# Kernel optimization log

Hardware: AMD Instinct MI355X
Metric: run time of the kernel (lower is better)

The kernel has to match this reference:

```python
import jax, jax.numpy as jnp
import numpy as np

B, S, D_MODEL, H, OUT = 32, 64, 256, 256, 10
N_POS = 64  # n_max_seq + 1


def _coordinate_map():
    i = jnp.arange(N_POS, dtype=jnp.float32)
    r = jnp.sqrt(jnp.float32(N_POS))
    c0 = (i / r - 2.0) / 2.0
    c1 = (jnp.mod(i, r) - 2.0) / 2.0
    coord = jnp.stack([c0, c1], axis=-1)            # [N_POS, 2]
    return jnp.broadcast_to(coord[None], (B, N_POS, 2))


def setup_inputs() -> dict:
    key = jax.random.key(0)
    ks = jax.random.split(key, 13)
    d_in = (D_MODEL + 2) * 3
    w = lambda k, i, o: jax.random.normal(k, (i, o), jnp.float32) * 0.02
    b = lambda k, o: jax.random.normal(k, (o,), jnp.float32) * 0.02
    return {
        'sentences': jax.random.normal(ks[0], (B, S, D_MODEL), jnp.float32),
        'coord': _coordinate_map(),
        'g_w1': w(ks[1], d_in, H), 'g_b1': b(ks[2], H),
        'g_w2': w(ks[3], H, H),    'g_b2': b(ks[4], H),
        'g_w3': w(ks[5], H, H),    'g_b3': b(ks[6], H),
        'f_w1': w(ks[7], H, H),    'f_b1': b(ks[8], H),
        'f_w2': w(ks[9], H, H),    'f_b2': b(ks[10], H),
        'f_w3': w(ks[11], H, OUT), 'f_b3': b(ks[12], OUT),
    }


def reference(sentences, coord, g_w1, g_b1, g_w2, g_b2, g_w3, g_b3,
              f_w1, f_b1, f_w2, f_b2, f_w3, f_b3):
    b, s, d = sentences.shape
    x = jnp.concatenate([sentences, coord[:b, :s, :]], axis=-1)   # [B,S,D+2]
    oi = jnp.broadcast_to(x[:, None, :, :], (b, s, s, d + 2))     # object_i[b,i,j]=x[b,j]
    oj = jnp.broadcast_to(x[:, :, None, :], (b, s, s, d + 2))     # object_j[b,i,j]=x[b,i]
    pairs = jnp.concatenate([oi, oj, oi * oj], axis=-1)           # [B,S,S,3*(D+2)]
    h = jax.nn.relu(jnp.einsum('bijk,kh->bijh', pairs, g_w1) + g_b1)
    h = jax.nn.relu(h @ g_w2 + g_b2)
    h = jax.nn.relu(h @ g_w3 + g_b3)
    rel = h.reshape(b, s * s, -1).sum(axis=1)                     # [B,H]
    y = jax.nn.relu(rel @ f_w1 + f_b1)
    y = jax.nn.relu(y @ f_w2 + f_b2)                              # Dropout: eval mode (identity)
    return y @ f_w3 + f_b3                                        # [B,OUT]
```

## Files before the change

### kernel.cpp

```cpp
#include <hip/hip_runtime.h>
#include <hip/hip_bf16.h>


typedef __attribute__((ext_vector_type(4))) float f32x4;
typedef __attribute__((ext_vector_type(16))) float f32x16;
typedef __attribute__((ext_vector_type(8))) short frag8;
typedef __attribute__((ext_vector_type(4))) unsigned u32x4;

__device__ __forceinline__ float bf2f(short s) {
  return __uint_as_float(((unsigned)(unsigned short)s) << 16);
}
__device__ __forceinline__ short f2bf(float f) {
  unsigned u = __float_as_uint(f);
  return (short)((u + 0x7fffu + ((u >> 16) & 1u)) >> 16);
}

__device__ __forceinline__ unsigned pk_bf16(float lo, float hi) {
#if __has_builtin(__builtin_amdgcn_cvt_pk_bf16_f32)
  return __builtin_bit_cast(unsigned, __builtin_amdgcn_cvt_pk_bf16_f32(lo, hi));
#else
  unsigned ul = __float_as_uint(lo), uh = __float_as_uint(hi);
  ul = (ul + 0x7fffu + ((ul >> 16) & 1u)) >> 16;
  uh = (uh + 0x7fffu + ((uh >> 16) & 1u)) & 0xffff0000u;
  return ul | uh;
#endif
}

__device__ __forceinline__ unsigned pk_mul_bf16(unsigned a, unsigned b) {
  float al = __uint_as_float(a << 16);
  float ah = __uint_as_float(a & 0xffff0000u);
  float bl = __uint_as_float(b << 16);
  float bh = __uint_as_float(b & 0xffff0000u);
  return pk_bf16(al * bl, ah * bh);
}

__device__ __forceinline__ frag8 pk_mul4(u32x4 a, u32x4 b) {
  u32x4 r;
#pragma unroll
  for (int t = 0; t < 4; t++) r[t] = pk_mul_bf16(a[t], b[t]);
  return __builtin_bit_cast(frag8, r);
}

#define KX 288

__global__ __launch_bounds__(256)
void prep(const float* __restrict__ sent, const float* __restrict__ coord,
          const float* __restrict__ g_w1, const float* __restrict__ g_w2,
          const float* __restrict__ g_w3,
          short* __restrict__ xb, short* __restrict__ Wab, short* __restrict__ Wc,
          short* __restrict__ W2t, short* __restrict__ W3t, float* __restrict__ rel) {
  __shared__ short tile[64 * 66];
  const int blk = blockIdx.x, t = threadIdx.x;

  if (blk < 288) {
    long idx0 = ((long)blk * 256 + t) * 8;
#pragma unroll
    for (int e = 0; e < 8; e++) {
      long idx = idx0 + e;
      int row = (int)(idx / KX), k = (int)(idx - (long)row * KX);
      float v = 0.f;
      if (k < 256)      v = sent[(size_t)row * 256 + k];
      else if (k < 258) v = coord[row * 2 + (k - 256)];
      xb[idx] = f2bf(v);
    }
    return;
  }

  const int nc = t & 63, r4 = t >> 6;
  if (blk < 328) {
    int tt = blk - 288, kt = tt >> 3, nt = tt & 7;
    int k0 = kt * 64, n0 = nt * 64;
    for (int p = 0; p < 16; p++) {
      int kl = p * 4 + r4, k = k0 + kl, n = n0 + nc;
      float v = 0.f;
      if (k < 258) {
        int row = (n < 256) ? k : 258 + k;
        int col = (n < 256) ? n : n - 256;
        v = g_w1[(size_t)row * 256 + col];
      }
      tile[kl * 66 + nc] = f2bf(v);
    }
    __syncthreads();
    for (int p = 0; p < 16; p++) {
      int nl = p * 4 + r4;
      if (k0 + nc < KX) Wab[(size_t)(n0 + nl) * KX + k0 + nc] = tile[nc * 66 + nl];
    }
    return;
  }
  if (blk < 348) {
    int tt = blk - 328, kt = tt >> 2, nt = tt & 3;
    int k0 = kt * 64, n0 = nt * 64;
    for (int p = 0; p < 16; p++) {
      int kl = p * 4 + r4, k = k0 + kl;
      float v = (k < 258) ? g_w1[(size_t)(516 + k) * 256 + n0 + nc] : 0.f;
      tile[kl * 66 + nc] = f2bf(v);
    }
    __syncthreads();
    for (int p = 0; p < 16; p++) {
      int nl = p * 4 + r4;
      if (k0 + nc < KX) Wc[(size_t)(n0 + nl) * KX + k0 + nc] = tile[nc * 66 + nl];
    }
    return;
  }
  if (blk < 380) {
    int tt = blk - 348;
    const float* W = (tt < 16) ? g_w2 : g_w3;
    short* Wt = (tt < 16) ? W2t : W3t;
    tt &= 15;
    int k0 = (tt >> 2) * 64, n0 = (tt & 3) * 64;
    for (int p = 0; p < 16; p++) {
      int kl = p * 4 + r4;
      tile[kl * 66 + nc] = f2bf(W[(size_t)(k0 + kl) * 256 + n0 + nc]);
    }
    __syncthreads();
    for (int p = 0; p < 16; p++) {
      int nl = p * 4 + r4;
      Wt[(size_t)(n0 + nl) * 256 + k0 + nc] = tile[nc * 66 + nl];
    }
    return;
  }
  {
    int bb = blk - 380;
    ((f32x4*)rel)[bb * 256 + t] = (f32x4){0.f, 0.f, 0.f, 0.f};
  }
}


__global__ __launch_bounds__(64)
void uv_gemm(const short* __restrict__ xb, const short* __restrict__ Wab,
             const float* __restrict__ g_b1, float* __restrict__ uv) {
  const int m0 = blockIdx.x * 64;
  const int n0 = blockIdx.y * 64;
  const int lane = threadIdx.x;
  const int q = lane >> 4, l16 = lane & 15;

  f32x4 acc[4][4];
#pragma unroll
  for (int mt = 0; mt < 4; mt++)
#pragma unroll
    for (int nt = 0; nt < 4; nt++) acc[mt][nt] = (f32x4){0.f, 0.f, 0.f, 0.f};

  for (int k0 = 0; k0 < KX; k0 += 32) {
    frag8 a[4], bb[4];
#pragma unroll
    for (int mt = 0; mt < 4; mt++)
      a[mt] = *(const frag8*)(xb + (size_t)(m0 + mt * 16 + l16) * KX + k0 + q * 8);
#pragma unroll
    for (int nt = 0; nt < 4; nt++)
      bb[nt] = *(const frag8*)(Wab + (size_t)(n0 + nt * 16 + l16) * KX + k0 + q * 8);
#pragma unroll
    for (int mt = 0; mt < 4; mt++)
#pragma unroll
      for (int nt = 0; nt < 4; nt++)
        acc[mt][nt] = __builtin_amdgcn_mfma_f32_16x16x32_bf16(a[mt], bb[nt], acc[mt][nt], 0, 0, 0);
  }
#pragma unroll
  for (int nt = 0; nt < 4; nt++) {
    int col = n0 + nt * 16 + l16;
    float bias = (col >= 256) ? g_b1[col - 256] : 0.f;
#pragma unroll
    for (int mt = 0; mt < 4; mt++) {
      int m = m0 + mt * 16 + q * 4;
#pragma unroll
      for (int r = 0; r < 4; r++)
        uv[(size_t)(m + r) * 512 + col] = acc[mt][nt][r] + bias;
    }
  }
}


#define ASH 152
#define A2OFF (128 * ASH)
#define LDS_SHORTS (2 * 128 * ASH)

__global__ __launch_bounds__(512, 4)
void relnet_main(const short* __restrict__ xb, const short* __restrict__ Wc,
                 const short* __restrict__ W2t, const short* __restrict__ W3t,
                 const float* __restrict__ uv, const float* __restrict__ g_b2,
                 const float* __restrict__ g_b3, float* __restrict__ rel) {
  __shared__ short lds[LDS_SHORTS];

  const int tid = threadIdx.x;
  const int bi = blockIdx.x;
  const int b = bi >> 5, ip = bi & 31;
  const int i0 = ip * 2;
  const int lane = tid & 63, wave = tid >> 6;
  const int l32 = lane & 31, half = lane >> 5;
  const int n0 = wave * 32;
  const int rowbase = b * 64;
  const int swr = l32 & 7;
  const int col = n0 + l32;
  const int cb = n0 >> 3;

  f32x16 acc[4];
#pragma unroll
  for (int mt = 0; mt < 4; mt++)
#pragma unroll
    for (int r = 0; r < 16; r++) acc[mt][r] = 0.f;

#pragma unroll
  for (int it = 0; it < 9; it++) {
    int idx = tid + it * 512;
    if (idx < 4352) {
      int j = idx / 34, c = idx - j * 34;
      int k = c * 8;
      u32x4 aj = *(const u32x4*)(xb + (size_t)(rowbase + (j & 63)) * KX + k);
      u32x4 ai = *(const u32x4*)(xb + (size_t)(rowbase + i0 + (j >> 6)) * KX + k);
      frag8 pr = pk_mul4(aj, ai);
      if (c < 18) *(frag8*)(&lds[j * ASH + k]) = pr;
      else        *(frag8*)(&lds[A2OFF + j * ASH + (k - 144)]) = pr;
    }
  }
  __syncthreads();

  {
    const short* wc = Wc + (size_t)(n0 + l32) * KX + half * 8;
    frag8 b0 = *(const frag8*)(wc);
#pragma unroll
    for (int ks = 0; ks < 17; ks++) {
      frag8 b1;
      if (ks < 16) b1 = *(const frag8*)(wc + (ks + 1) * 16);
      frag8 a[4];
#pragma unroll
      for (int mt = 0; mt < 4; mt++) {
        int base = (ks < 9) ? ((mt * 32 + l32) * ASH + ks * 16 + half * 8)
                            : (A2OFF + (mt * 32 + l32) * ASH + (ks - 9) * 16 + half * 8);
        a[mt] = *(const frag8*)(&lds[base]);
      }
#pragma unroll
      for (int mt = 0; mt < 4; mt++)
        acc[mt] = __builtin_amdgcn_mfma_f32_32x32x16_bf16(a[mt], b0, acc[mt], 0, 0, 0);
      b0 = b1;
    }
  }
  __syncthreads();

  {
    const float* ub = uv + (size_t)rowbase * 512;
    float vv0 = uv[(size_t)(rowbase + i0) * 512 + 256 + col];
    float vv1 = uv[(size_t)(rowbase + i0 + 1) * 512 + 256 + col];
#pragma unroll
    for (int mt = 0; mt < 4; mt++) {
      float vv = (mt < 2) ? vv0 : vv1;
#pragma unroll
      for (int r = 0; r < 16; r += 2) {
        int rb0 = (r & 3) + 8 * (r >> 2) + 4 * half;
        int jm0 = (mt & 1) * 32 + rb0;
        float x0 = fmaxf(acc[mt][r]     + ub[(size_t)jm0 * 512 + col] + vv, 0.f);
        float x1 = fmaxf(acc[mt][r + 1] + ub[(size_t)(jm0 + 1) * 512 + col] + vv, 0.f);
        unsigned pk = pk_bf16(x0, x1);
        int m0r = mt * 32 + rb0;
        int sw0 = (r & 3) + 4 * half;
        lds[m0r * 256 + (((cb + (l32 >> 3)) ^ sw0) << 3) + (l32 & 7)] = (short)(pk & 0xffffu);
        lds[(m0r + 1) * 256 + (((cb + (l32 >> 3)) ^ (sw0 + 1)) << 3) + (l32 & 7)] = (short)(pk >> 16);
      }
#pragma unroll
      for (int r = 0; r < 16; r++) acc[mt][r] = 0.f;
    }
  }
  __syncthreads();

  {
    const short* w2 = W2t + (size_t)(n0 + l32) * 256 + half * 8;
    frag8 b0 = *(const frag8*)(w2);
#pragma unroll
    for (int ks = 0; ks < 16; ks++) {
      frag8 b1;
      if (ks < 15) b1 = *(const frag8*)(w2 + (ks + 1) * 16);
      frag8 a[4];
#pragma unroll
      for (int mt = 0; mt < 4; mt++)
        a[mt] = *(const frag8*)(&lds[(mt * 32 + l32) * 256 + (((2 * ks + half) ^ swr) << 3)]);
#pragma unroll
      for (int mt = 0; mt < 4; mt++)
        acc[mt] = __builtin_amdgcn_mfma_f32_32x32x16_bf16(a[mt], b0, acc[mt], 0, 0, 0);
      b0 = b1;
    }
  }
  __syncthreads();

  {
    float b2 = g_b2[col];
#pragma unroll
    for (int mt = 0; mt < 4; mt++) {
#pragma unroll
      for (int r = 0; r < 16; r += 2) {
        int rb0 = (r & 3) + 8 * (r >> 2) + 4 * half;
        float x0 = fmaxf(acc[mt][r] + b2, 0.f);
        float x1 = fmaxf(acc[mt][r + 1] + b2, 0.f);
        unsigned pk = pk_bf16(x0, x1);
        int m0r = mt * 32 + rb0;
        int sw0 = (r & 3) + 4 * half;
        lds[m0r * 256 + (((cb + (l32 >> 3)) ^ sw0) << 3) + (l32 & 7)] = (short)(pk & 0xffffu);
        lds[(m0r + 1) * 256 + (((cb + (l32 >> 3)) ^ (sw0 + 1)) << 3) + (l32 & 7)] = (short)(pk >> 16);
      }
#pragma unroll
      for (int r = 0; r < 16; r++) acc[mt][r] = 0.f;
    }
  }
  __syncthreads();

  {
    const short* w3 = W3t + (size_t)(n0 + l32) * 256 + half * 8;
    frag8 b0 = *(const frag8*)(w3);
#pragma unroll
    for (int ks = 0; ks < 16; ks++) {
      frag8 b1;
      if (ks < 15) b1 = *(const frag8*)(w3 + (ks + 1) * 16);
      frag8 a[4];
#pragma unroll
      for (int mt = 0; mt < 4; mt++)
        a[mt] = *(const frag8*)(&lds[(mt * 32 + l32) * 256 + (((2 * ks + half) ^ swr) << 3)]);
#pragma unroll
      for (int mt = 0; mt < 4; mt++)
        acc[mt] = __builtin_amdgcn_mfma_f32_32x32x16_bf16(a[mt], b0, acc[mt], 0, 0, 0);
      b0 = b1;
    }
  }
  {
    float b3 = g_b3[col];
    float s = 0.f;
#pragma unroll
    for (int mt = 0; mt < 4; mt++)
#pragma unroll
      for (int r = 0; r < 16; r++)
        s += fmaxf(acc[mt][r] + b3, 0.f);
    s += __shfl_xor(s, 32, 64);
    if (half == 0) atomicAdd(&rel[b * 256 + col], s);
  }
}

__global__ __launch_bounds__(256)
void fnet(const float* __restrict__ rel, const float* __restrict__ f_w1,
          const float* __restrict__ f_b1, const float* __restrict__ f_w2,
          const float* __restrict__ f_b2, const float* __restrict__ f_w3,
          const float* __restrict__ f_b3, float* __restrict__ out) {
  int b = blockIdx.x, t = threadIdx.x;
  __shared__ float y0[256], y1[256], y2[256];
  y0[t] = rel[b * 256 + t];
  __syncthreads();
  float s = f_b1[t];
#pragma unroll 8
  for (int k = 0; k < 256; k++) s += y0[k] * f_w1[k * 256 + t];
  y1[t] = fmaxf(s, 0.f);
  __syncthreads();
  s = f_b2[t];
#pragma unroll 8
  for (int k = 0; k < 256; k++) s += y1[k] * f_w2[k * 256 + t];
  y2[t] = fmaxf(s, 0.f);
  __syncthreads();
  if (t < 10) {
    float s2 = f_b3[t];
#pragma unroll 8
    for (int k = 0; k < 256; k++) s2 += y2[k] * f_w3[k * 10 + t];
    out[b * 10 + t] = s2;
  }
}

extern "C" void kernel_launch(void* const* d_in, const int* in_sizes, int n_in,
                              void* d_out, int out_size, void* d_ws, size_t ws_size,
                              hipStream_t stream) {
  const float* sent  = (const float*)d_in[0];
  const float* coord = (const float*)d_in[1];
  const float* g_w1  = (const float*)d_in[2];
  const float* g_b1  = (const float*)d_in[3];
  const float* g_w2  = (const float*)d_in[4];
  const float* g_b2  = (const float*)d_in[5];
  const float* g_w3  = (const float*)d_in[6];
  const float* g_b3  = (const float*)d_in[7];
  const float* f_w1  = (const float*)d_in[8];
  const float* f_b1  = (const float*)d_in[9];
  const float* f_w2  = (const float*)d_in[10];
  const float* f_b2  = (const float*)d_in[11];
  const float* f_w3  = (const float*)d_in[12];
  const float* f_b3  = (const float*)d_in[13];
  float* out = (float*)d_out;

  char* ws = (char*)d_ws;
  size_t off = 0;
  auto alloc = [&](size_t bytes) {
    char* p = ws + off;
    off += (bytes + 255) & ~(size_t)255;
    return p;
  };
  short* xb  = (short*)alloc((size_t)2048 * KX * 2);
  short* Wab = (short*)alloc((size_t)512 * KX * 2);
  short* Wc  = (short*)alloc((size_t)256 * KX * 2);
  short* W2t = (short*)alloc((size_t)256 * 256 * 2);
  short* W3t = (short*)alloc((size_t)256 * 256 * 2);
  float* uv  = (float*)alloc((size_t)2048 * 512 * 4);
  float* rel = (float*)alloc((size_t)32 * 256 * 4);

  prep<<<388, 256, 0, stream>>>(sent, coord, g_w1, g_w2, g_w3, xb, Wab, Wc, W2t, W3t, rel);
  uv_gemm<<<dim3(32, 8), 64, 0, stream>>>(xb, Wab, g_b1, uv);
  relnet_main<<<1024, 512, 0, stream>>>(xb, Wc, W2t, W3t, uv, g_b2, g_b3, rel);
  fnet<<<32, 256, 0, stream>>>(rel, f_w1, f_b1, f_w2, f_b2, f_w3, f_b3, out);
}
```

Measured before the change: 198.8 us.

## Retile relnet_main to one i-row per block with 64x64 wave tiles

Each relnet_main block now handles a single query row i (64 pairs) with 256 threads and 4 waves, instead of two rows (128 pairs) with 512 threads and 8 waves. Each wave computes a 64x64 tile as 2x2 32x32 MFMA tiles rather than a 128x32 tile, and the LDS A tile becomes 64 rows with a 280-short stride, dropping the split two-region layout. Grid doubles to 2048 blocks and launch bounds change to (256,3). The aim is better occupancy, a smaller LDS footprint and more B-fragment reuse per A load. The cost is that weights are reloaded per block twice as often.

```diff
diff --git a/kernel.cpp b/kernel.cpp
--- a/kernel.cpp
+++ b/kernel.cpp
@@ -169,11 +169,10 @@
 }
 
 
-#define ASH 152
-#define A2OFF (128 * ASH)
-#define LDS_SHORTS (2 * 128 * ASH)
-
-__global__ __launch_bounds__(512, 4)
+#define ASH 280
+#define LDS_SHORTS (64 * ASH)
+
+__global__ __launch_bounds__(256, 3)
 void relnet_main(const short* __restrict__ xb, const short* __restrict__ Wc,
                  const short* __restrict__ W2t, const short* __restrict__ W3t,
                  const float* __restrict__ uv, const float* __restrict__ g_b2,
@@ -182,149 +181,171 @@
 
   const int tid = threadIdx.x;
   const int bi = blockIdx.x;
-  const int b = bi >> 5, ip = bi & 31;
-  const int i0 = ip * 2;
+  const int b = bi >> 6, i = bi & 63;
   const int lane = tid & 63, wave = tid >> 6;
   const int l32 = lane & 31, half = lane >> 5;
-  const int n0 = wave * 32;
+  const int n0 = wave * 64;
   const int rowbase = b * 64;
   const int swr = l32 & 7;
-  const int col = n0 + l32;
-  const int cb = n0 >> 3;
-
-  f32x16 acc[4];
-#pragma unroll
-  for (int mt = 0; mt < 4; mt++)
-#pragma unroll
-    for (int r = 0; r < 16; r++) acc[mt][r] = 0.f;
-
-#pragma unroll
-  for (int it = 0; it < 9; it++) {
-    int idx = tid + it * 512;
-    if (idx < 4352) {
+
+  f32x16 acc[2][2];
+#pragma unroll
+  for (int mt = 0; mt < 2; mt++)
+#pragma unroll
+    for (int nt = 0; nt < 2; nt++)
+#pragma unroll
+      for (int r = 0; r < 16; r++) acc[mt][nt][r] = 0.f;
+
+  {
+    const short* xi = xb + (size_t)(rowbase + i) * KX;
+    for (int idx = tid; idx < 64 * 34; idx += 256) {
       int j = idx / 34, c = idx - j * 34;
       int k = c * 8;
-      u32x4 aj = *(const u32x4*)(xb + (size_t)(rowbase + (j & 63)) * KX + k);
-      u32x4 ai = *(const u32x4*)(xb + (size_t)(rowbase + i0 + (j >> 6)) * KX + k);
-      frag8 pr = pk_mul4(aj, ai);
-      if (c < 18) *(frag8*)(&lds[j * ASH + k]) = pr;
-      else        *(frag8*)(&lds[A2OFF + j * ASH + (k - 144)]) = pr;
-    }
-  }
-  __syncthreads();
-
-  {
-    const short* wc = Wc + (size_t)(n0 + l32) * KX + half * 8;
-    frag8 b0 = *(const frag8*)(wc);
+      u32x4 aj = *(const u32x4*)(xb + (size_t)(rowbase + j) * KX + k);
+      u32x4 ai = *(const u32x4*)(xi + k);
+      *(frag8*)(&lds[j * ASH + k]) = pk_mul4(aj, ai);
+    }
+  }
+  __syncthreads();
+
+  {
+    const short* wc0 = Wc + (size_t)(n0 + l32) * KX + half * 8;
+    const short* wc1 = Wc + (size_t)(n0 + 32 + l32) * KX + half * 8;
+    frag8 b0 = *(const frag8*)(wc0);
+    frag8 b1 = *(const frag8*)(wc1);
 #pragma unroll
     for (int ks = 0; ks < 17; ks++) {
-      frag8 b1;
-      if (ks < 16) b1 = *(const frag8*)(wc + (ks + 1) * 16);
-      frag8 a[4];
-#pragma unroll
-      for (int mt = 0; mt < 4; mt++) {
-        int base = (ks < 9) ? ((mt * 32 + l32) * ASH + ks * 16 + half * 8)
-                            : (A2OFF + (mt * 32 + l32) * ASH + (ks - 9) * 16 + half * 8);
-        a[mt] = *(const frag8*)(&lds[base]);
-      }
-#pragma unroll
-      for (int mt = 0; mt < 4; mt++)
-        acc[mt] = __builtin_amdgcn_mfma_f32_32x32x16_bf16(a[mt], b0, acc[mt], 0, 0, 0);
-      b0 = b1;
+      frag8 bn0, bn1;
+      if (ks < 16) {
+        bn0 = *(const frag8*)(wc0 + (ks + 1) * 16);
+        bn1 = *(const frag8*)(wc1 + (ks + 1) * 16);
+      }
+      frag8 a[2];
+#pragma unroll
+      for (int mt = 0; mt < 2; mt++)
+        a[mt] = *(const frag8*)(&lds[(mt * 32 + l32) * ASH + ks * 16 + half * 8]);
+#pragma unroll
+      for (int mt = 0; mt < 2; mt++) {
+        acc[mt][0] = __builtin_amdgcn_mfma_f32_32x32x16_bf16(a[mt], b0, acc[mt][0], 0, 0, 0);
+        acc[mt][1] = __builtin_amdgcn_mfma_f32_32x32x16_bf16(a[mt], b1, acc[mt][1], 0, 0, 0);
+      }
+      b0 = bn0; b1 = bn1;
     }
   }
   __syncthreads();
 
   {
     const float* ub = uv + (size_t)rowbase * 512;
-    float vv0 = uv[(size_t)(rowbase + i0) * 512 + 256 + col];
-    float vv1 = uv[(size_t)(rowbase + i0 + 1) * 512 + 256 + col];
-#pragma unroll
-    for (int mt = 0; mt < 4; mt++) {
-      float vv = (mt < 2) ? vv0 : vv1;
+    const float* vp = uv + (size_t)(rowbase + i) * 512 + 256;
+#pragma unroll
+    for (int nt = 0; nt < 2; nt++) {
+      int col = n0 + nt * 32 + l32;
+      int cb = (n0 + nt * 32) >> 3;
+      float vv = vp[col];
+#pragma unroll
+      for (int mt = 0; mt < 2; mt++) {
+#pragma unroll
+        for (int r = 0; r < 16; r += 2) {
+          int rb0 = (r & 3) + 8 * (r >> 2) + 4 * half;
+          int m0r = mt * 32 + rb0;
+          float x0 = fmaxf(acc[mt][nt][r]     + ub[(size_t)m0r * 512 + col] + vv, 0.f);
+          float x1 = fmaxf(acc[mt][nt][r + 1] + ub[(size_t)(m0r + 1) * 512 + col] + vv, 0.f);
+          unsigned pk = pk_bf16(x0, x1);
+          int sw0 = (r & 3) + 4 * half;
+          lds[m0r * 256 + (((cb + (l32 >> 3)) ^ sw0) << 3) + (l32 & 7)] = (short)(pk & 0xffffu);
+          lds[(m0r + 1) * 256 + (((cb + (l32 >> 3)) ^ (sw0 + 1)) << 3) + (l32 & 7)] = (short)(pk >> 16);
+        }
+#pragma unroll
+        for (int r = 0; r < 16; r++) acc[mt][nt][r] = 0.f;
+      }
+    }
+  }
+  __syncthreads();
+
+  {
+    const short* w20 = W2t + (size_t)(n0 + l32) * 256 + half * 8;
+    const short* w21 = W2t + (size_t)(n0 + 32 + l32) * 256 + half * 8;
+    frag8 b0 = *(const frag8*)(w20);
+    frag8 b1 = *(const frag8*)(w21);
+#pragma unroll
+    for (int ks = 0; ks < 16; ks++) {
+      frag8 bn0, bn1;
+      if (ks < 15) {
+        bn0 = *(const frag8*)(w20 + (ks + 1) * 16);
+        bn1 = *(const frag8*)(w21 + (ks + 1) * 16);
+      }
+      frag8 a[2];
+#pragma unroll
+      for (int mt = 0; mt < 2; mt++)
+        a[mt] = *(const frag8*)(&lds[(mt * 32 + l32) * 256 + (((2 * ks + half) ^ swr) << 3)]);
+#pragma unroll
+      for (int mt = 0; mt < 2; mt++) {
+        acc[mt][0] = __builtin_amdgcn_mfma_f32_32x32x16_bf16(a[mt], b0, acc[mt][0], 0, 0, 0);
+        acc[mt][1] = __builtin_amdgcn_mfma_f32_32x32x16_bf16(a[mt], b1, acc[mt][1], 0, 0, 0);
+      }
+      b0 = bn0; b1 = bn1;
+    }
+  }
+  __syncthreads();
+
+#pragma unroll
+  for (int nt = 0; nt < 2; nt++) {
+    int col = n0 + nt * 32 + l32;
+    int cb = (n0 + nt * 32) >> 3;
+    float b2 = g_b2[col];
+#pragma unroll
+    for (int mt = 0; mt < 2; mt++) {
 #pragma unroll
       for (int r = 0; r < 16; r += 2) {
         int rb0 = (r & 3) + 8 * (r >> 2) + 4 * half;
-        int jm0 = (mt & 1) * 32 + rb0;
-        float x0 = fmaxf(acc[mt][r]     + ub[(size_t)jm0 * 512 + col] + vv, 0.f);
-        float x1 = fmaxf(acc[mt][r + 1] + ub[(size_t)(jm0 + 1) * 512 + col] + vv, 0.f);
+        int m0r = mt * 32 + rb0;
+        float x0 = fmaxf(acc[mt][nt][r] + b2, 0.f);
+        float x1 = fmaxf(acc[mt][nt][r + 1] + b2, 0.f);
         unsigned pk = pk_bf16(x0, x1);
-        int m0r = mt * 32 + rb0;
         int sw0 = (r & 3) + 4 * half;
         lds[m0r * 256 + (((cb + (l32 >> 3)) ^ sw0) << 3) + (l32 & 7)] = (short)(pk & 0xffffu);
         lds[(m0r + 1) * 256 + (((cb + (l32 >> 3)) ^ (sw0 + 1)) << 3) + (l32 & 7)] = (short)(pk >> 16);
       }
 #pragma unroll
-      for (int r = 0; r < 16; r++) acc[mt][r] = 0.f;
-    }
-  }
-  __syncthreads();
-
-  {
-    const short* w2 = W2t + (size_t)(n0 + l32) * 256 + half * 8;
-    frag8 b0 = *(const frag8*)(w2);
+      for (int r = 0; r < 16; r++) acc[mt][nt][r] = 0.f;
+    }
+  }
+  __syncthreads();
+
+  {
+    const short* w30 = W3t + (size_t)(n0 + l32) * 256 + half * 8;
+    const short* w31 = W3t + (size_t)(n0 + 32 + l32) * 256 + half * 8;
+    frag8 b0 = *(const frag8*)(w30);
+    frag8 b1 = *(const frag8*)(w31);
 #pragma unroll
     for (int ks = 0; ks < 16; ks++) {
-      frag8 b1;
-      if (ks < 15) b1 = *(const frag8*)(w2 + (ks + 1) * 16);
-      frag8 a[4];
-#pragma unroll
-      for (int mt = 0; mt < 4; mt++)
+      frag8 bn0, bn1;
+      if (ks < 15) {
+        bn0 = *(const frag8*)(w30 + (ks + 1) * 16);
+        bn1 = *(const frag8*)(w31 + (ks + 1) * 16);
+      }
+      frag8 a[2];
+#pragma unroll
+      for (int mt = 0; mt < 2; mt++)
         a[mt] = *(const frag8*)(&lds[(mt * 32 + l32) * 256 + (((2 * ks + half) ^ swr) << 3)]);
 #pragma unroll
-      for (int mt = 0; mt < 4; mt++)
-        acc[mt] = __builtin_amdgcn_mfma_f32_32x32x16_bf16(a[mt], b0, acc[mt], 0, 0, 0);
-      b0 = b1;
-    }
-  }
-  __syncthreads();
-
-  {
-    float b2 = g_b2[col];
-#pragma unroll
-    for (int mt = 0; mt < 4; mt++) {
-#pragma unroll
-      for (int r = 0; r < 16; r += 2) {
-        int rb0 = (r & 3) + 8 * (r >> 2) + 4 * half;
-        float x0 = fmaxf(acc[mt][r] + b2, 0.f);
-        float x1 = fmaxf(acc[mt][r + 1] + b2, 0.f);
-        unsigned pk = pk_bf16(x0, x1);
-        int m0r = mt * 32 + rb0;
-        int sw0 = (r & 3) + 4 * half;
-        lds[m0r * 256 + (((cb + (l32 >> 3)) ^ sw0) << 3) + (l32 & 7)] = (short)(pk & 0xffffu);
-        lds[(m0r + 1) * 256 + (((cb + (l32 >> 3)) ^ (sw0 + 1)) << 3) + (l32 & 7)] = (short)(pk >> 16);
-      }
-#pragma unroll
-      for (int r = 0; r < 16; r++) acc[mt][r] = 0.f;
-    }
-  }
-  __syncthreads();
-
-  {
-    const short* w3 = W3t + (size_t)(n0 + l32) * 256 + half * 8;
-    frag8 b0 = *(const frag8*)(w3);
-#pragma unroll
-    for (int ks = 0; ks < 16; ks++) {
-      frag8 b1;
-      if (ks < 15) b1 = *(const frag8*)(w3 + (ks + 1) * 16);
-      frag8 a[4];
-#pragma unroll
-      for (int mt = 0; mt < 4; mt++)
-        a[mt] = *(const frag8*)(&lds[(mt * 32 + l32) * 256 + (((2 * ks + half) ^ swr) << 3)]);
-#pragma unroll
-      for (int mt = 0; mt < 4; mt++)
-        acc[mt] = __builtin_amdgcn_mfma_f32_32x32x16_bf16(a[mt], b0, acc[mt], 0, 0, 0);
-      b0 = b1;
-    }
-  }
-  {
+      for (int mt = 0; mt < 2; mt++) {
+        acc[mt][0] = __builtin_amdgcn_mfma_f32_32x32x16_bf16(a[mt], b0, acc[mt][0], 0, 0, 0);
+        acc[mt][1] = __builtin_amdgcn_mfma_f32_32x32x16_bf16(a[mt], b1, acc[mt][1], 0, 0, 0);
+      }
+      b0 = bn0; b1 = bn1;
+    }
+  }
+#pragma unroll
+  for (int nt = 0; nt < 2; nt++) {
+    int col = n0 + nt * 32 + l32;
     float b3 = g_b3[col];
     float s = 0.f;
 #pragma unroll
-    for (int mt = 0; mt < 4; mt++)
+    for (int mt = 0; mt < 2; mt++)
 #pragma unroll
       for (int r = 0; r < 16; r++)
-        s += fmaxf(acc[mt][r] + b3, 0.f);
+        s += fmaxf(acc[mt][nt][r] + b3, 0.f);
     s += __shfl_xor(s, 32, 64);
     if (half == 0) atomicAdd(&rel[b * 256 + col], s);
   }
@@ -393,6 +414,6 @@
 
   prep<<<388, 256, 0, stream>>>(sent, coord, g_w1, g_w2, g_w3, xb, Wab, Wc, W2t, W3t, rel);
   uv_gemm<<<dim3(32, 8), 64, 0, stream>>>(xb, Wab, g_b1, uv);
-  relnet_main<<<1024, 512, 0, stream>>>(xb, Wc, W2t, W3t, uv, g_b2, g_b3, rel);
+  relnet_main<<<2048, 256, 0, stream>>>(xb, Wc, W2t, W3t, uv, g_b2, g_b3, rel);
   fnet<<<32, 256, 0, stream>>>(rel, f_w1, f_b1, f_w2, f_b2, f_w3, f_b3, out);
 }
```

New measurement: 230.2 us. 1.16x slower.
